# Performance work log

Measured on AMD Instinct MI355X. Metric: run time of the kernel, lower is better.

Reference implementation:

```python
import jax, jax.numpy as jnp
import numpy as np

B, N, K = 2, 8192, 16          # batch, points, ED_nsample
SA_C, DG_C = 128, 1024         # SA_conv_out, DG_conv_out
CAT_C = SA_C + SA_C // 4 + 4   # 164 channels into head


def _conv1(W, b, x):
    # 1x1 Conv1d: W [out,in], x [B,in,N]
    return jnp.einsum('oc,bcn->bon', W, x) + b[None, :, None]


def _bn_relu(x, g, be):
    # BatchNorm1d (training-mode batch stats) + ReLU, x [B,C,N]
    m = x.mean(axis=(0, 2), keepdims=True)
    v = x.var(axis=(0, 2), keepdims=True)
    return jax.nn.relu((x - m) * jax.lax.rsqrt(v + 1e-5) * g[None, :, None] + be[None, :, None])


def setup_inputs() -> dict:
    key = jax.random.key(0)
    ks = jax.random.split(key, 32)
    w = lambda k, s: jax.random.normal(k, s, jnp.float32) * 0.05
    p = {}
    p['pointcloud'] = jax.random.normal(ks[0], (B, N, 3), jnp.float32)
    p['h1'] = jax.random.normal(ks[1], (B, SA_C, N), jnp.float32)
    p['h2'] = jax.random.normal(ks[2], (B, DG_C, N), jnp.float32)
    p['numpoints'] = N
    # DG head convs 1024->256->64->32
    p['DG_w1'], p['DG_b1'] = w(ks[3], (256, DG_C)), jnp.zeros(256, jnp.float32)
    p['DG_g1'], p['DG_be1'] = jnp.ones(256, jnp.float32), jnp.zeros(256, jnp.float32)
    p['DG_w2'], p['DG_b2'] = w(ks[4], (64, 256)), jnp.zeros(64, jnp.float32)
    p['DG_g2'], p['DG_be2'] = jnp.ones(64, jnp.float32), jnp.zeros(64, jnp.float32)
    p['DG_w3'], p['DG_b3'] = w(ks[5], (SA_C // 4, 64)), jnp.zeros(SA_C // 4, jnp.float32)
    p['DG_g3'], p['DG_be3'] = jnp.ones(SA_C // 4, jnp.float32), jnp.zeros(SA_C // 4, jnp.float32)
    # ED MLP 3->4->4
    p['ED_w1'], p['ED_b1'] = w(ks[6], (3, 4)), jnp.zeros(4, jnp.float32)
    p['ED_w2'], p['ED_b2'] = w(ks[7], (4, 4)), jnp.zeros(4, jnp.float32)
    # head convs 164->512->256->128
    p['C_w1'], p['C_b1'] = w(ks[8], (512, CAT_C)), jnp.zeros(512, jnp.float32)
    p['C_g1'], p['C_be1'] = jnp.ones(512, jnp.float32), jnp.zeros(512, jnp.float32)
    p['C_w2'], p['C_b2'] = w(ks[9], (256, 512)), jnp.zeros(256, jnp.float32)
    p['C_g2'], p['C_be2'] = jnp.ones(256, jnp.float32), jnp.zeros(256, jnp.float32)
    p['C_w3'], p['C_b3'] = w(ks[10], (128, 256)), jnp.zeros(128, jnp.float32)
    p['C_g3'], p['C_be3'] = jnp.ones(128, jnp.float32), jnp.zeros(128, jnp.float32)
    return p


def reference(pointcloud, h1, h2, numpoints,
              DG_w1, DG_b1, DG_g1, DG_be1, DG_w2, DG_b2, DG_g2, DG_be2,
              DG_w3, DG_b3, DG_g3, DG_be3,
              ED_w1, ED_b1, ED_w2, ED_b2,
              C_w1, C_b1, C_g1, C_be1, C_w2, C_b2, C_g2, C_be2,
              C_w3, C_b3, C_g3, C_be3):
    xyz = pointcloud[..., :3]
    # DG branch head
    h2p = _bn_relu(_conv1(DG_w1, DG_b1, h2), DG_g1, DG_be1)
    h2p = _bn_relu(_conv1(DG_w2, DG_b2, h2p), DG_g2, DG_be2)
    h2p = _bn_relu(_conv1(DG_w3, DG_b3, h2p), DG_g3, DG_be3)
    # ED branch: brute-force knn on squared distances
    sq = jnp.sum(xyz * xyz, axis=-1)                               # [B,N]
    d = sq[:, :, None] + sq[:, None, :] - 2.0 * jnp.einsum('bnd,bmd->bnm', xyz, xyz)
    _, idx = jax.lax.top_k(-d, K)                                  # [B,N,K]
    nbr = jax.vmap(lambda pts, i: pts[i])(xyz, idx)                # [B,N,K,3]
    c = nbr - nbr.mean(axis=2, keepdims=True)
    cov = jnp.einsum('bnkd,bnke->bnde', c, c) / K                  # [B,N,3,3]
    ev = jnp.linalg.eigvalsh(cov)                                  # [B,N,3] ascending
    h3 = jax.nn.relu(ev @ ED_w1 + ED_b1) @ ED_w2 + ED_b2           # [B,N,4]
    # fuse and head
    z = jnp.concatenate([h1, h2p, jnp.transpose(h3, (0, 2, 1))], axis=1)
    z = _bn_relu(_conv1(C_w1, C_b1, z), C_g1, C_be1)
    z = _bn_relu(_conv1(C_w2, C_b2, z), C_g2, C_be2)
    z = _bn_relu(_conv1(C_w3, C_b3, z), C_g3, C_be3)
    return xyz, z
```

## Files before the change

kernel.cpp:

```cpp
#include <hip/hip_runtime.h>

#define NPTS 8192
#define BATCH 2

typedef __attribute__((ext_vector_type(8))) __bf16 bf16x8;
typedef __attribute__((ext_vector_type(4))) float f32x4;
typedef unsigned int u32;

__device__ inline unsigned short f2bf(float x) {
    unsigned u = __float_as_uint(x);
    u += 0x7fffu + ((u >> 16) & 1u);
    return (unsigned short)(u >> 16);
}
__device__ inline unsigned pack32(float d, unsigned idx) {
    unsigned u = __float_as_uint(d);
    u ^= ((unsigned)((int)u >> 31)) | 0x80000000u;
    return (u & 0xFFFFE000u) | idx;
}
__device__ inline unsigned bitonic64u(unsigned key, int lane) {
#pragma unroll
    for (int k = 2; k <= 64; k <<= 1) {
#pragma unroll
        for (int j = k >> 1; j > 0; j >>= 1) {
            unsigned o = __shfl_xor(key, j, 64);
            bool tmin = (((lane & k) == 0) == ((lane & j) == 0));
            key = ((o < key) == tmin) ? o : key;
        }
    }
    return key;
}
__device__ inline void ins16(unsigned& key, unsigned c, int lane) {
    unsigned prev = __shfl_up(key, 1, 64);
    if (lane == 0) prev = 0u;
    unsigned mx = prev > c ? prev : c;
    key = mx < key ? mx : key;
}
__device__ inline float distf(float4 q, float4 p) {
    return fmaf(-2.f, fmaf(q.z, p.z, fmaf(q.y, p.y, q.x * p.x)), q.w + p.w);
}

__global__ __launch_bounds__(256) void prep_presplit(
    const float* __restrict__ pc, float* __restrict__ oxyz, float4* __restrict__ pq,
    const float* __restrict__ W0, const float* __restrict__ W1,
    const float* __restrict__ W2, const float* __restrict__ W3,
    const float* __restrict__ W4, const float* __restrict__ W5,
    unsigned short* __restrict__ wsp) {
    int bx = blockIdx.x, tid = threadIdx.x;
    if (bx < 64) {
        int t = bx * 256 + tid;
        float x = pc[t * 3 + 0], y = pc[t * 3 + 1], z = pc[t * 3 + 2];
        oxyz[t * 3 + 0] = x; oxyz[t * 3 + 1] = y; oxyz[t * 3 + 2] = z;
        pq[t] = make_float4(x, y, z, fmaf(z, z, fmaf(y, y, x * x)));
        return;
    }
    int pb = bx - 64;
    const float* W; int O, C, OP; size_t off; int base;
    if (pb < 1024)      { W = W0; O = 256; C = 1024; OP = 256; off = 0;       base = 0; }
    else if (pb < 1152) { W = W1; O =  64; C =  256; OP = 128; off = 524288;  base = 1024; }
    else if (pb < 1184) { W = W2; O =  32; C =   64; OP = 128; off = 589824;  base = 1152; }
    else if (pb < 1568) { W = W3; O = 512; C =  164; OP = 512; off = 606208;  base = 1184; }
    else if (pb < 2080) { W = W4; O = 256; C =  512; OP = 256; off = 802816;  base = 1568; }
    else                { W = W5; O = 128; C =  256; OP = 128; off = 1064960; base = 2080; }
    unsigned short* dst = wsp + off;
    int t = (pb - base) * 256 + tid;
    int kk = t & 31;
    int o = (t >> 5) % OP;
    int kt = t / (OP * 32);
    int c = kt * 32 + kk;
    float x = (o < O && c < C) ? W[o * C + c] : 0.f;
    unsigned short hb = f2bf(x);
    float hf = __uint_as_float((unsigned)hb << 16);
    unsigned short lb = f2bf(x - hf);
    int s = kk >> 3, pos = kk & 7;
    int sst = s ^ ((o >> 1) & 3);
    dst[((size_t)(kt * 2) * OP + o) * 32 + sst * 8 + pos] = hb;
    dst[((size_t)(kt * 2 + 1) * OP + o) * 32 + sst * 8 + pos] = lb;
}

template <int MODE>
__global__ __launch_bounds__(256, 2) void mfma_gemm(
    const unsigned short* __restrict__ Wsp, const float* __restrict__ bias,
    const float* __restrict__ X, float* __restrict__ out,
    int O, int C, int OP, int nK,
    const float2* __restrict__ stats,
    const float* __restrict__ h1, const float* __restrict__ h3,
    const float2* __restrict__ stats3) {
    const int N = NPTS;
    int tid = threadIdx.x;
    int lane = tid & 63, w = tid >> 6;
    int wm = w >> 1, wn = w & 1;
    int b = blockIdx.z, n0 = blockIdx.x * 64, o0 = blockIdx.y * 128;

    __shared__ __align__(16) unsigned char lds[26624];
    unsigned char* WHp = lds;
    unsigned char* WLp = lds + 8192;
    unsigned char* XHp = lds + 16384;
    unsigned char* XLp = lds + 21504;

    f32x4 acc[4][2];
#pragma unroll
    for (int i = 0; i < 4; ++i)
#pragma unroll
        for (int j = 0; j < 2; ++j) acc[i][j] = (f32x4){0.f, 0.f, 0.f, 0.f};

    for (int kt = 0; kt < nK; ++kt) {
        int c0 = kt * 32;
#pragma unroll
        for (int comp = 0; comp < 2; ++comp) {
            const unsigned short* gb = Wsp + ((size_t)(kt * 2 + comp) * OP + o0) * 32;
            unsigned char* lb = comp ? WLp : WHp;
#pragma unroll
            for (int i = 0; i < 2; ++i) {
                int chunk = w + i * 4;
                __builtin_amdgcn_global_load_lds(
                    (const __attribute__((address_space(1))) u32*)(gb + chunk * 512 + lane * 8),
                    (__attribute__((address_space(3))) u32*)(lb + chunk * 1024),
                    16, 0, 0);
            }
        }
        {
            int n = n0 + lane;
            float v[8];
#pragma unroll
            for (int i = 0; i < 8; ++i) {
                int c = c0 + w * 8 + i;
                float x = 0.f;
                if (MODE == 0) {
                    if (c < C) x = X[((size_t)(b * C + c)) * N + n];
                } else if (MODE == 1) {
                    if (c < C) {
                        float2 st = stats[c];
                        float y = X[((size_t)(b * C + c)) * N + n];
                        x = fmaxf(fmaf(y, st.x, st.y), 0.f);
                    }
                } else {
                    if (c < 128) {
                        x = h1[((size_t)(b * 128 + c)) * N + n];
                    } else if (c < 160) {
                        float2 st = stats3[c - 128];
                        float y = X[((size_t)(b * 32 + (c - 128))) * N + n];
                        x = fmaxf(fmaf(y, st.x, st.y), 0.f);
                    } else if (c < 164) {
                        x = h3[((size_t)(b * 4 + (c - 160))) * N + n];
                    }
                }
                v[i] = x;
            }
            union { bf16x8 s; unsigned short u[8]; } hh, ll;
#pragma unroll
            for (int i = 0; i < 8; ++i) {
                unsigned short hb = f2bf(v[i]);
                float hf = __uint_as_float((unsigned)hb << 16);
                unsigned short lb = f2bf(v[i] - hf);
                hh.u[i] = hb; ll.u[i] = lb;
            }
            *(bf16x8*)(XHp + lane * 80 + w * 16) = hh.s;
            *(bf16x8*)(XLp + lane * 80 + w * 16) = ll.s;
        }
        __syncthreads();
        {
            int koff = (lane >> 4) * 16;
            int rb = wn * 32 + (lane & 15);
            bf16x8 bh[2], bl[2];
#pragma unroll
            for (int ni = 0; ni < 2; ++ni) {
                bh[ni] = *(const bf16x8*)(XHp + (rb + ni * 16) * 80 + koff);
                bl[ni] = *(const bf16x8*)(XLp + (rb + ni * 16) * 80 + koff);
            }
#pragma unroll
            for (int mi = 0; mi < 4; ++mi) {
                int ra = wm * 64 + mi * 16 + (lane & 15);
                int sw = koff ^ ((((unsigned)ra >> 1) & 3) * 16);
                bf16x8 ah = *(const bf16x8*)(WHp + ra * 64 + sw);
                bf16x8 al = *(const bf16x8*)(WLp + ra * 64 + sw);
#pragma unroll
                for (int ni = 0; ni < 2; ++ni) {
                    acc[mi][ni] = __builtin_amdgcn_mfma_f32_16x16x32_bf16(ah, bh[ni], acc[mi][ni], 0, 0, 0);
                    acc[mi][ni] = __builtin_amdgcn_mfma_f32_16x16x32_bf16(ah, bl[ni], acc[mi][ni], 0, 0, 0);
                    acc[mi][ni] = __builtin_amdgcn_mfma_f32_16x16x32_bf16(al, bh[ni], acc[mi][ni], 0, 0, 0);
                }
            }
        }
        __syncthreads();
    }
    int col = lane & 15, rq = lane >> 4;
#pragma unroll
    for (int mi = 0; mi < 4; ++mi) {
#pragma unroll
        for (int j = 0; j < 4; ++j) {
            int o = o0 + wm * 64 + mi * 16 + rq * 4 + j;
            if (o < O) {
                float bs = bias[o];
                float* po = out + ((size_t)(b * O + o)) * N + n0 + wn * 32 + col;
#pragma unroll
                for (int ni = 0; ni < 2; ++ni) po[ni * 16] = acc[mi][ni][j] + bs;
            }
        }
    }
}

__global__ __launch_bounds__(256) void stats_kernel(const float* __restrict__ X,
                                                    const float* __restrict__ g,
                                                    const float* __restrict__ be,
                                                    float2* __restrict__ st, int C) {
    const int N = NPTS;
    int c = blockIdx.x;
    int tid = threadIdx.x;
    float s1 = 0.f, s2 = 0.f;
    for (int b = 0; b < BATCH; ++b) {
        const float* p = X + (size_t)(b * C + c) * N;
        for (int n = tid * 4; n < N; n += 1024) {
            float4 v = *(const float4*)(p + n);
            s1 += v.x + v.y + v.z + v.w;
            s2 += v.x * v.x + v.y * v.y + v.z * v.z + v.w * v.w;
        }
    }
    __shared__ float r1[256], r2[256];
    r1[tid] = s1; r2[tid] = s2;
    __syncthreads();
    for (int off = 128; off > 0; off >>= 1) {
        if (tid < off) { r1[tid] += r1[tid + off]; r2[tid] += r2[tid + off]; }
        __syncthreads();
    }
    if (tid == 0) {
        float inv = 1.f / (BATCH * N);
        float m = r1[0] * inv;
        float var = r2[0] * inv - m * m;
        float sc = g[c] * rsqrtf(var + 1e-5f);
        st[c] = make_float2(sc, be[c] - m * sc);
    }
}

__global__ __launch_bounds__(256) void knn_eig_kernel(
    const float4* __restrict__ pq,
    const float* __restrict__ ew1, const float* __restrict__ eb1,
    const float* __restrict__ ew2, const float* __restrict__ eb2,
    float* __restrict__ h3) {
    int wv = threadIdx.x >> 6;
    int lane = threadIdx.x & 63;
    int sg = blockIdx.x * 4 + wv;
    int b = sg >> 12;
    int iloc = (sg & 4095) << 1;
    const float4* pqb = pq + (size_t)b * NPTS;
    float4 Q0 = pqb[iloc + 0], Q1 = pqb[iloc + 1];

    float4 p = pqb[lane];
    unsigned k0 = bitonic64u(pack32(distf(Q0, p), lane), lane);
    unsigned k1 = bitonic64u(pack32(distf(Q1, p), lane), lane);
    unsigned tk0 = (unsigned)__builtin_amdgcn_readlane((int)k0, 15);
    unsigned tk1 = (unsigned)__builtin_amdgcn_readlane((int)k1, 15);

    float4 A = pqb[64 + lane];
    float4 B = pqb[128 + lane];
    for (int it = 1; it + 1 < 128; it += 2) {
        int tbA = it * 64, tbB = tbA + 64;
        int t3 = (it + 3 < 128) ? it + 3 : 0;
        float4 Cx = pqb[(it + 2) * 64 + lane];
        float4 Dx = pqb[t3 * 64 + lane];
        unsigned cA0 = pack32(distf(Q0, A), tbA + lane);
        unsigned cA1 = pack32(distf(Q1, A), tbA + lane);
        unsigned cB0 = pack32(distf(Q0, B), tbB + lane);
        unsigned cB1 = pack32(distf(Q1, B), tbB + lane);
        unsigned long long mA0 = __ballot(cA0 < tk0), mB0 = __ballot(cB0 < tk0);
        unsigned long long mA1 = __ballot(cA1 < tk1), mB1 = __ballot(cB1 < tk1);
        if (mA0 | mA1 | mB0 | mB1) {
            while (mA0) {
                int L = __ffsll((long long)mA0) - 1; mA0 &= mA0 - 1;
                ins16(k0, (unsigned)__builtin_amdgcn_readlane((int)cA0, L), lane);
            }
            while (mB0) {
                int L = __ffsll((long long)mB0) - 1; mB0 &= mB0 - 1;
                ins16(k0, (unsigned)__builtin_amdgcn_readlane((int)cB0, L), lane);
            }
            while (mA1) {
                int L = __ffsll((long long)mA1) - 1; mA1 &= mA1 - 1;
                ins16(k1, (unsigned)__builtin_amdgcn_readlane((int)cA1, L), lane);
            }
            while (mB1) {
                int L = __ffsll((long long)mB1) - 1; mB1 &= mB1 - 1;
                ins16(k1, (unsigned)__builtin_amdgcn_readlane((int)cB1, L), lane);
            }
            tk0 = (unsigned)__builtin_amdgcn_readlane((int)k0, 15);
            tk1 = (unsigned)__builtin_amdgcn_readlane((int)k1, 15);
        }
        A = Cx; B = Dx;
    }
    {
        int tbA = 127 * 64;
        unsigned cA0 = pack32(distf(Q0, A), tbA + lane);
        unsigned cA1 = pack32(distf(Q1, A), tbA + lane);
        unsigned long long mA0 = __ballot(cA0 < tk0);
        unsigned long long mA1 = __ballot(cA1 < tk1);
        while (mA0) {
            int L = __ffsll((long long)mA0) - 1; mA0 &= mA0 - 1;
            ins16(k0, (unsigned)__builtin_amdgcn_readlane((int)cA0, L), lane);
        }
        while (mA1) {
            int L = __ffsll((long long)mA1) - 1; mA1 &= mA1 - 1;
            ins16(k1, (unsigned)__builtin_amdgcn_readlane((int)cA1, L), lane);
        }
    }

    int g = lane >> 4, r = lane & 15;
    unsigned j0 = ((unsigned)__shfl((int)k0, r, 64)) & 8191u;
    unsigned j1 = ((unsigned)__shfl((int)k1, r, 64)) & 8191u;
    unsigned nj = ((g & 1) == 0) ? j0 : j1;

    float4 nb = pqb[nj];
    float sx = nb.x, sy = nb.y, sz = nb.z;
#pragma unroll
    for (int m = 1; m < 16; m <<= 1) {
        sx += __shfl_xor(sx, m, 64);
        sy += __shfl_xor(sy, m, 64);
        sz += __shfl_xor(sz, m, 64);
    }
    const float i16 = 1.f / 16.f;
    float cx = nb.x - sx * i16, cy = nb.y - sy * i16, cz = nb.z - sz * i16;
    float xx = cx * cx, xy = cx * cy, xz = cx * cz, yy = cy * cy, yz = cy * cz, zz = cz * cz;
#pragma unroll
    for (int m = 1; m < 16; m <<= 1) {
        xx += __shfl_xor(xx, m, 64); xy += __shfl_xor(xy, m, 64); xz += __shfl_xor(xz, m, 64);
        yy += __shfl_xor(yy, m, 64); yz += __shfl_xor(yz, m, 64); zz += __shfl_xor(zz, m, 64);
    }
    float a11 = xx * i16, a12 = xy * i16, a13 = xz * i16,
          a22 = yy * i16, a23 = yz * i16, a33 = zz * i16;
    float q = (a11 + a22 + a33) * (1.f / 3.f);
    float p1 = a12 * a12 + a13 * a13 + a23 * a23;
    float b11 = a11 - q, b22 = a22 - q, b33 = a33 - q;
    float p2 = b11 * b11 + b22 * b22 + b33 * b33 + 2.f * p1;
    float pr = sqrtf(p2 * (1.f / 6.f));
    float ipv = (p2 > 1e-32f) ? (1.f / pr) : 0.f;
    float detB = b11 * (b22 * b33 - a23 * a23) - a12 * (a12 * b33 - a23 * a13) +
                 a13 * (a12 * a23 - b22 * a13);
    float r3 = 0.5f * detB * ipv * ipv * ipv;
    r3 = fminf(1.f, fmaxf(-1.f, r3));
    float phi = acosf(r3) * (1.f / 3.f);
    float e1 = q + 2.f * pr * cosf(phi);
    float e3 = q + 2.f * pr * cosf(phi + 2.0943951023931953f);
    float e2 = 3.f * q - e1 - e3;
    float ev0 = e3, ev1 = e2, ev2 = e1;
    float h[4], o[4];
#pragma unroll
    for (int kk = 0; kk < 4; ++kk)
        h[kk] = fmaxf(eb1[kk] + ev0 * ew1[kk] + ev1 * ew1[4 + kk] + ev2 * ew1[8 + kk], 0.f);
#pragma unroll
    for (int kk = 0; kk < 4; ++kk)
        o[kk] = eb2[kk] + h[0] * ew2[kk] + h[1] * ew2[4 + kk] + h[2] * ew2[8 + kk] +
                h[3] * ew2[12 + kk];
    int ipt = iloc + (g & 1);
    if (r == 0 && g < 2) {
#pragma unroll
        for (int kk = 0; kk < 4; ++kk) h3[(b * 4 + kk) * NPTS + ipt] = o[kk];
    }
}

__global__ __launch_bounds__(256) void final_kernel(const float* __restrict__ X,
                                                    const float2* __restrict__ st,
                                                    float* __restrict__ out) {
    int idx4 = blockIdx.x * 256 + threadIdx.x;
    int base = idx4 * 4;
    int c = (base >> 13) & 127;
    float2 s = st[c];
    float4 v = *(const float4*)(X + base);
    v.x = fmaxf(fmaf(v.x, s.x, s.y), 0.f);
    v.y = fmaxf(fmaf(v.y, s.x, s.y), 0.f);
    v.z = fmaxf(fmaf(v.z, s.x, s.y), 0.f);
    v.w = fmaxf(fmaf(v.w, s.x, s.y), 0.f);
    *(float4*)(out + base) = v;
}

extern "C" void kernel_launch(void* const* d_in, const int* in_sizes, int n_in,
                              void* d_out, int out_size, void* d_ws, size_t ws_size,
                              hipStream_t stream) {
    const float* pc    = (const float*)d_in[0];
    const float* h1    = (const float*)d_in[1];
    const float* h2    = (const float*)d_in[2];
    const float* DG_w1 = (const float*)d_in[4];
    const float* DG_b1 = (const float*)d_in[5];
    const float* DG_g1 = (const float*)d_in[6];
    const float* DG_be1= (const float*)d_in[7];
    const float* DG_w2 = (const float*)d_in[8];
    const float* DG_b2 = (const float*)d_in[9];
    const float* DG_g2 = (const float*)d_in[10];
    const float* DG_be2= (const float*)d_in[11];
    const float* DG_w3 = (const float*)d_in[12];
    const float* DG_b3 = (const float*)d_in[13];
    const float* DG_g3 = (const float*)d_in[14];
    const float* DG_be3= (const float*)d_in[15];
    const float* ED_w1 = (const float*)d_in[16];
    const float* ED_b1 = (const float*)d_in[17];
    const float* ED_w2 = (const float*)d_in[18];
    const float* ED_b2 = (const float*)d_in[19];
    const float* C_w1  = (const float*)d_in[20];
    const float* C_b1  = (const float*)d_in[21];
    const float* C_g1  = (const float*)d_in[22];
    const float* C_be1 = (const float*)d_in[23];
    const float* C_w2  = (const float*)d_in[24];
    const float* C_b2  = (const float*)d_in[25];
    const float* C_g2  = (const float*)d_in[26];
    const float* C_be2 = (const float*)d_in[27];
    const float* C_w3  = (const float*)d_in[28];
    const float* C_b3  = (const float*)d_in[29];
    const float* C_g3  = (const float*)d_in[30];
    const float* C_be3 = (const float*)d_in[31];

    float* ws = (float*)d_ws;
    float* A  = ws;
    float* Bb = ws + (8l << 20);
    float* Cc = ws + (12l << 20);
    float* H3 = ws + (14l << 20);
    float4* PQ = (float4*)(H3 + 65536);
    float2* ST = (float2*)(H3 + 131072);
    unsigned short* WSP = (unsigned short*)(H3 + 131072 + 2560);

    const size_t W1SP = 0;
    const size_t W2SP = 524288;
    const size_t W3SP = 589824;
    const size_t C1SP = 606208;
    const size_t C2SP = 802816;
    const size_t C3SP = 1064960;

    float* outxyz = (float*)d_out;
    float* outz   = (float*)d_out + BATCH * NPTS * 3;

    prep_presplit<<<2272, 256, 0, stream>>>(pc, outxyz, PQ,
                                            DG_w1, DG_w2, DG_w3, C_w1, C_w2, C_w3, WSP);

    mfma_gemm<0><<<dim3(128, 2, 2), 256, 0, stream>>>(WSP + W1SP, DG_b1, h2, A, 256, 1024, 256, 32,
                                                      nullptr, nullptr, nullptr, nullptr);
    stats_kernel<<<256, 256, 0, stream>>>(A, DG_g1, DG_be1, ST + 0, 256);
    mfma_gemm<1><<<dim3(128, 1, 2), 256, 0, stream>>>(WSP + W2SP, DG_b2, A, Bb, 64, 256, 128, 8,
                                                      ST + 0, nullptr, nullptr, nullptr);
    stats_kernel<<<64, 256, 0, stream>>>(Bb, DG_g2, DG_be2, ST + 256, 64);
    mfma_gemm<1><<<dim3(128, 1, 2), 256, 0, stream>>>(WSP + W3SP, DG_b3, Bb, Cc, 32, 64, 128, 2,
                                                      ST + 256, nullptr, nullptr, nullptr);
    stats_kernel<<<32, 256, 0, stream>>>(Cc, DG_g3, DG_be3, ST + 320, 32);

    knn_eig_kernel<<<2048, 256, 0, stream>>>(PQ, ED_w1, ED_b1, ED_w2, ED_b2, H3);

    mfma_gemm<2><<<dim3(128, 4, 2), 256, 0, stream>>>(WSP + C1SP, C_b1, Cc, A, 512, 164, 512, 6,
                                                      nullptr, h1, H3, ST + 320);
    stats_kernel<<<512, 256, 0, stream>>>(A, C_g1, C_be1, ST + 352, 512);
    mfma_gemm<1><<<dim3(128, 2, 2), 256, 0, stream>>>(WSP + C2SP, C_b2, A, Bb, 256, 512, 256, 16,
                                                      ST + 352, nullptr, nullptr, nullptr);
    stats_kernel<<<256, 256, 0, stream>>>(Bb, C_g2, C_be2, ST + 864, 256);
    mfma_gemm<1><<<dim3(128, 1, 2), 256, 0, stream>>>(WSP + C3SP, C_b3, Bb, Cc, 128, 256, 128, 8,
                                                      ST + 864, nullptr, nullptr, nullptr);
    stats_kernel<<<128, 256, 0, stream>>>(Cc, C_g3, C_be3, ST + 1120, 128);

    final_kernel<<<2048, 256, 0, stream>>>(Cc, ST + 1120, outz);
}
```

Before: 309.3 us.

## Prefetch next K-tile activations in GEMM and fuse final stats with BN-ReLU

```diff
diff --git a/kernel.cpp b/kernel.cpp
--- a/kernel.cpp
+++ b/kernel.cpp
@@ -90,6 +90,7 @@
     int lane = tid & 63, w = tid >> 6;
     int wm = w >> 1, wn = w & 1;
     int b = blockIdx.z, n0 = blockIdx.x * 64, o0 = blockIdx.y * 128;
+    int n = n0 + lane;
 
     __shared__ __align__(16) unsigned char lds[26624];
     unsigned char* WHp = lds;
@@ -103,6 +104,25 @@
 #pragma unroll
         for (int j = 0; j < 2; ++j) acc[i][j] = (f32x4){0.f, 0.f, 0.f, 0.f};
 
+    float xcur[8], xnxt[8];
+
+    auto loadx = [&](int kt, float (&dst)[8]) {
+#pragma unroll
+        for (int i = 0; i < 8; ++i) {
+            int c = kt * 32 + w * 8 + i;
+            float x = 0.f;
+            if (MODE == 0 || MODE == 1) {
+                if (c < C) x = X[((size_t)(b * C + c)) * N + n];
+            } else {
+                if (c < 128)       x = h1[((size_t)(b * 128 + c)) * N + n];
+                else if (c < 160)  x = X[((size_t)(b * 32 + (c - 128))) * N + n];
+                else if (c < 164)  x = h3[((size_t)(b * 4 + (c - 160))) * N + n];
+            }
+            dst[i] = x;
+        }
+    };
+
+    loadx(0, xcur);
     for (int kt = 0; kt < nK; ++kt) {
         int c0 = kt * 32;
 #pragma unroll
@@ -119,44 +139,31 @@
             }
         }
         {
-            int n = n0 + lane;
-            float v[8];
+            union { bf16x8 s; unsigned short u[8]; } hh, ll;
 #pragma unroll
             for (int i = 0; i < 8; ++i) {
                 int c = c0 + w * 8 + i;
-                float x = 0.f;
-                if (MODE == 0) {
-                    if (c < C) x = X[((size_t)(b * C + c)) * N + n];
-                } else if (MODE == 1) {
+                float x = xcur[i];
+                if (MODE == 1) {
                     if (c < C) {
                         float2 st = stats[c];
-                        float y = X[((size_t)(b * C + c)) * N + n];
-                        x = fmaxf(fmaf(y, st.x, st.y), 0.f);
+                        x = fmaxf(fmaf(x, st.x, st.y), 0.f);
                     }
-                } else {
-                    if (c < 128) {
-                        x = h1[((size_t)(b * 128 + c)) * N + n];
-                    } else if (c < 160) {
+                } else if (MODE == 2) {
+                    if (c >= 128 && c < 160) {
                         float2 st = stats3[c - 128];
-                        float y = X[((size_t)(b * 32 + (c - 128))) * N + n];
-                        x = fmaxf(fmaf(y, st.x, st.y), 0.f);
-                    } else if (c < 164) {
-                        x = h3[((size_t)(b * 4 + (c - 160))) * N + n];
+                        x = fmaxf(fmaf(x, st.x, st.y), 0.f);
                     }
                 }
-                v[i] = x;
-            }
-            union { bf16x8 s; unsigned short u[8]; } hh, ll;
-#pragma unroll
-            for (int i = 0; i < 8; ++i) {
-                unsigned short hb = f2bf(v[i]);
+                unsigned short hb = f2bf(x);
                 float hf = __uint_as_float((unsigned)hb << 16);
-                unsigned short lb = f2bf(v[i] - hf);
+                unsigned short lb = f2bf(x - hf);
                 hh.u[i] = hb; ll.u[i] = lb;
             }
             *(bf16x8*)(XHp + lane * 80 + w * 16) = hh.s;
             *(bf16x8*)(XLp + lane * 80 + w * 16) = ll.s;
         }
+        if (kt + 1 < nK) loadx(kt + 1, xnxt);
         __syncthreads();
         {
             int koff = (lane >> 4) * 16;
@@ -182,6 +189,10 @@
             }
         }
         __syncthreads();
+        if (kt + 1 < nK) {
+#pragma unroll
+            for (int i = 0; i < 8; ++i) xcur[i] = xnxt[i];
+        }
     }
     int col = lane & 15, rq = lane >> 4;
 #pragma unroll
@@ -228,6 +239,54 @@
         float var = r2[0] * inv - m * m;
         float sc = g[c] * rsqrtf(var + 1e-5f);
         st[c] = make_float2(sc, be[c] - m * sc);
+    }
+}
+
+__global__ __launch_bounds__(256) void stats_final_kernel(const float* __restrict__ X,
+                                                          const float* __restrict__ g,
+                                                          const float* __restrict__ be,
+                                                          float* __restrict__ outz) {
+    const int N = NPTS;
+    const int C = 128;
+    int c = blockIdx.x;
+    int tid = threadIdx.x;
+    float s1 = 0.f, s2 = 0.f;
+    for (int b = 0; b < BATCH; ++b) {
+        const float* p = X + (size_t)(b * C + c) * N;
+        for (int n = tid * 4; n < N; n += 1024) {
+            float4 v = *(const float4*)(p + n);
+            s1 += v.x + v.y + v.z + v.w;
+            s2 += v.x * v.x + v.y * v.y + v.z * v.z + v.w * v.w;
+        }
+    }
+    __shared__ float r1[256], r2[256];
+    __shared__ float2 stv;
+    r1[tid] = s1; r2[tid] = s2;
+    __syncthreads();
+    for (int off = 128; off > 0; off >>= 1) {
+        if (tid < off) { r1[tid] += r1[tid + off]; r2[tid] += r2[tid + off]; }
+        __syncthreads();
+    }
+    if (tid == 0) {
+        float inv = 1.f / (BATCH * N);
+        float m = r1[0] * inv;
+        float var = r2[0] * inv - m * m;
+        float sc = g[c] * rsqrtf(var + 1e-5f);
+        stv = make_float2(sc, be[c] - m * sc);
+    }
+    __syncthreads();
+    float2 s = stv;
+    for (int b = 0; b < BATCH; ++b) {
+        const float* p = X + (size_t)(b * C + c) * N;
+        float* q = outz + (size_t)(b * C + c) * N;
+        for (int nn = tid * 4; nn < N; nn += 1024) {
+            float4 v = *(const float4*)(p + nn);
+            v.x = fmaxf(fmaf(v.x, s.x, s.y), 0.f);
+            v.y = fmaxf(fmaf(v.y, s.x, s.y), 0.f);
+            v.z = fmaxf(fmaf(v.z, s.x, s.y), 0.f);
+            v.w = fmaxf(fmaf(v.w, s.x, s.y), 0.f);
+            *(float4*)(q + nn) = v;
+        }
     }
 }
 
@@ -352,21 +411,6 @@
 #pragma unroll
         for (int kk = 0; kk < 4; ++kk) h3[(b * 4 + kk) * NPTS + ipt] = o[kk];
     }
-}
-
-__global__ __launch_bounds__(256) void final_kernel(const float* __restrict__ X,
-                                                    const float2* __restrict__ st,
-                                                    float* __restrict__ out) {
-    int idx4 = blockIdx.x * 256 + threadIdx.x;
-    int base = idx4 * 4;
-    int c = (base >> 13) & 127;
-    float2 s = st[c];
-    float4 v = *(const float4*)(X + base);
-    v.x = fmaxf(fmaf(v.x, s.x, s.y), 0.f);
-    v.y = fmaxf(fmaf(v.y, s.x, s.y), 0.f);
-    v.z = fmaxf(fmaf(v.z, s.x, s.y), 0.f);
-    v.w = fmaxf(fmaf(v.w, s.x, s.y), 0.f);
-    *(float4*)(out + base) = v;
 }
 
 extern "C" void kernel_launch(void* const* d_in, const int* in_sizes, int n_in,
@@ -446,7 +490,6 @@
     stats_kernel<<<256, 256, 0, stream>>>(Bb, C_g2, C_be2, ST + 864, 256);
     mfma_gemm<1><<<dim3(128, 1, 2), 256, 0, stream>>>(WSP + C3SP, C_b3, Bb, Cc, 128, 256, 128, 8,
                                                       ST + 864, nullptr, nullptr, nullptr);
-    stats_kernel<<<128, 256, 0, stream>>>(Cc, C_g3, C_be3, ST + 1120, 128);
-
-    final_kernel<<<2048, 256, 0, stream>>>(Cc, ST + 1120, outz);
-}
+
+    stats_final_kernel<<<128, 256, 0, stream>>>(Cc, C_g3, C_be3, outz);
+}
```

Result: faster. 287.1 us (-7.2%).
